# Performance work log

Hardware: AMD Instinct MI355X
Metric: run time of the kernel (lower is better)

Reference implementation:

```python
import jax, jax.numpy as jnp
import numpy as np

N_QUBITS = 14
LATENT = 14
DEPTH = 4
BATCH = 256
DIM = 1 << N_QUBITS  # 16384 amplitudes

# PennyLane convention: wire 0 is the most-significant bit of the flat state index.
_idx = np.arange(DIM)
_bits = (_idx[None, :] >> (N_QUBITS - 1 - np.arange(N_QUBITS)[:, None])) & 1  # [n_qubits, DIM]
_parity = np.sum(_bits[:-1] * _bits[1:], axis=0) % 2  # adjacent-pair CZ chain parity
CZ_SIGNS = jnp.asarray(1.0 - 2.0 * _parity, dtype=jnp.complex64)  # [DIM]
Z_SIGNS = jnp.asarray(1 - 2 * _bits[:LATENT], dtype=jnp.float32)  # [LATENT, DIM]


def _rx(t):
    c = jnp.cos(0.5 * t) + 0j
    s = -1j * jnp.sin(0.5 * t)
    m = jnp.stack([jnp.stack([c, s], -1), jnp.stack([s, c], -1)], -2)
    return m.astype(jnp.complex64)


def _ry(t):
    c = jnp.cos(0.5 * t)
    s = jnp.sin(0.5 * t)
    m = jnp.stack([jnp.stack([c, -s], -1), jnp.stack([s, c], -1)], -2)
    return m.astype(jnp.complex64)


def _rz(t):
    e = jnp.exp(-0.5j * t.astype(jnp.complex64))
    z = jnp.zeros_like(e)
    m = jnp.stack([jnp.stack([e, z], -1), jnp.stack([z, jnp.conj(e)], -1)], -2)
    return m.astype(jnp.complex64)


def _apply_1q(state, mat, wire):
    # state: [B, DIM]; mat: [2,2] (shared) or [B,2,2] (per-sample)
    B = state.shape[0]
    left = 1 << wire
    right = 1 << (N_QUBITS - wire - 1)
    st = state.reshape(B, left, 2, right)
    if mat.ndim == 3:
        st = jnp.einsum('bij,bajc->baic', mat, st)
    else:
        st = jnp.einsum('ij,bajc->baic', mat, st)
    return st.reshape(B, DIM)


def setup_inputs() -> dict:
    key = jax.random.key(0)
    k1, k2, k3, k4 = jax.random.split(key, 4)
    conditioning = jax.random.normal(k1, (BATCH, LATENT), dtype=jnp.float32)
    lim = 1.0 / np.sqrt(LATENT)
    W_enc = jax.random.uniform(k2, (N_QUBITS, LATENT), jnp.float32, -lim, lim)
    b_enc = jax.random.uniform(k3, (N_QUBITS,), jnp.float32, -lim, lim)
    # TorchLayer default init: U(0, 2*pi)
    weights = jax.random.uniform(k4, (DEPTH, N_QUBITS, 3), jnp.float32, 0.0, 2.0 * np.pi)
    return {"conditioning": conditioning, "W_enc": W_enc, "b_enc": b_enc, "weights": weights}


def reference(conditioning, W_enc, b_enc, weights):
    # encode: Linear + SiLU -> per-wire rotation angles [B, n_qubits]
    emb = conditioning @ W_enc.T + b_enc
    emb = emb * jax.nn.sigmoid(emb)
    B = emb.shape[0]

    state = jnp.zeros((B, DIM), jnp.complex64).at[:, 0].set(1.0)

    # angle encoding: RX(v) then RY(v) on each wire (per-sample gates)
    for w in range(N_QUBITS):
        v = emb[:, w]
        U = jnp.einsum('bij,bjk->bik', _ry(v), _rx(v))  # [B,2,2]
        state = _apply_1q(state, U, w)

    # variational layers: RZ, RX, RY per wire (shared gates), then CZ chain
    for d in range(DEPTH):
        for w in range(N_QUBITS):
            p = weights[d, w]
            U = _ry(p[2]) @ _rx(p[1]) @ _rz(p[0])  # [2,2]
            state = _apply_1q(state, U, w)
        state = state * CZ_SIGNS  # all adjacent CZs fused into one diagonal

    probs = state.real ** 2 + state.imag ** 2  # [B, DIM]
    latent = probs @ Z_SIGNS.T  # <Z_w> for w in range(LATENT) -> [B, LATENT]

    # F.layer_norm over last dim, no affine params
    mu = jnp.mean(latent, axis=-1, keepdims=True)
    var = jnp.var(latent, axis=-1, keepdims=True)
    return (latent - mu) / jnp.sqrt(var + 1e-5)
```

## Files before the change

### kernel.cpp

```cpp
#include <hip/hip_runtime.h>
#include <math.h>

#define NQ    14
#define DIM   16384
#define DEPTH 4

typedef __attribute__((ext_vector_type(2))) float f2;
typedef __attribute__((ext_vector_type(4))) float f4;

__device__ __forceinline__ f2 cmul(f2 a, f2 b) {
    return (f2){a.x*b.x - a.y*b.y, a.x*b.y + a.y*b.x};
}
__device__ __forceinline__ f2 cmac2(f2 x, f2 u, f2 us, f2 y, f2 v, f2 vs) {
    f2 r = x.xx * u;
    r += x.yy * us;
    r += y.xx * v;
    r += y.yy * vs;
    return r;
}


template<int CTRL>
__device__ __forceinline__ f2 dpp2(f2 v) {
    union U { f2 f; int i[2]; } u, r;
    u.f = v;
    r.i[0] = __builtin_amdgcn_update_dpp(0, u.i[0], CTRL, 0xF, 0xF, true);
    r.i[1] = __builtin_amdgcn_update_dpp(0, u.i[1], CTRL, 0xF, 0xF, true);
    return r.f;
}
template<int XB> __device__ __forceinline__ f2 lxchg(f2 v);
template<> __device__ __forceinline__ f2 lxchg<1>(f2 v) { return dpp2<0xB1>(v); }
template<> __device__ __forceinline__ f2 lxchg<2>(f2 v) { return dpp2<0x4E>(v); }
template<> __device__ __forceinline__ f2 lxchg<8>(f2 v) { return dpp2<0x128>(v); }

template<int MASK>
__device__ __forceinline__ void reg_gate(f2 a[16], const f4* G) {
    f4 g0 = G[0], g1 = G[1], g2 = G[2], g3 = G[3];
    #pragma unroll
    for (int l = 0; l < 16; ++l) {
        if (l & MASK) continue;
        const int j = l | MASK;
        f2 x = a[l], y = a[j];
        a[l] = cmac2(x, g0.xy, g0.zw, y, g1.xy, g1.zw);
        a[j] = cmac2(x, g2.xy, g2.zw, y, g3.xy, g3.zw);
    }
}

template<int XB>
__device__ __forceinline__ void lane_gate(f2 a[16], const f4* G, int t) {
    const bool hi = (t & XB) != 0;
    f4 c1 = G[hi ? 3 : 0];
    f4 c2 = G[hi ? 2 : 1];
    #pragma unroll
    for (int l = 0; l < 16; ++l) {
        f2 p = lxchg<XB>(a[l]);
        a[l] = cmac2(a[l], c1.xy, c1.zw, p, c2.xy, c2.zw);
    }
}

__device__ __forceinline__ void cz_A(f2 a[16], int t) {
    const int n = t & 63, w = t >> 6;
    const int pT = (__popc(w & (w >> 1)) + __popc(n & (n >> 1)) + ((n & 1) & (w >> 3))) & 1;
    const float F0 = pT ? -1.f : 1.f;
    const float F1 = (pT ^ ((n >> 5) & 1)) ? -1.f : 1.f;
    #pragma unroll
    for (int l = 0; l < 16; ++l) {
        float s = (l & 1) ? F1 : F0;
        if (__popc(l & (l >> 1)) & 1) s = -s;
        a[l] *= s;
    }
}

__device__ __forceinline__ void cz_B(f2 a[16], int t) {
    const int n = t & 63, w = t >> 6;
    const int n0 = n & 1, n1 = (n >> 1) & 1, n2 = (n >> 2) & 1;
    const int n3 = (n >> 3) & 1, n4 = (n >> 4) & 1, n5 = (n >> 5) & 1;
    const int pT = ((n2 & n4) ^ (n4 & n0) ^ (n0 & n5) ^ (n5 & n1) ^ (n1 & n3)
                    ^ (n3 & (w & 1)) ^ (__popc(w & (w >> 1)) & 1));
    const float F0 = pT ? -1.f : 1.f;
    const float F1 = (pT ^ n2) ? -1.f : 1.f;
    #pragma unroll
    for (int l = 0; l < 16; ++l) {
        float s = (l & 8) ? F1 : F0;
        if (__popc(l & (l >> 1)) & 1) s = -s;
        a[l] *= s;
    }
}

__global__ __launch_bounds__(1024)
void qlg_kernel(const float* __restrict__ cond,
                const float* __restrict__ Wenc,
                const float* __restrict__ benc,
                const float* __restrict__ wts,
                float* __restrict__ out)
{
    __shared__ f2 st[DIM];
    __shared__ f4 gates[DEPTH][NQ][4];
    __shared__ f2 qv[NQ][2];
    __shared__ f2 Phi[128];
    __shared__ f2 Plo[128];
    __shared__ float embS[NQ];
    __shared__ float wred[16][NQ];
    __shared__ float lat[NQ];

    const int b = blockIdx.x;
    const int t = threadIdx.x;
    const int n = t & 63, w = t >> 6;
    const int bB = (w << 10)
                 | (((n >> 3) & 1) << 5) | (((n >> 1) & 1) << 4)
                 | (((n >> 5) & 1) << 3) | ((n & 1) << 2)
                 | (((n >> 4) & 1) << 1) | ((n >> 2) & 1);

    if (t < NQ) {
        float s = benc[t];
        #pragma unroll
        for (int k = 0; k < NQ; ++k) s += cond[b*NQ + k] * Wenc[t*NQ + k];
        embS[t] = s / (1.0f + __expf(-s));
    }
    if (t >= 64 && t < 64 + DEPTH*NQ) {
        const int gi = t - 64;
        const int d = gi / NQ, ww = gi % NQ;
        const float p0 = wts[(d*NQ + ww)*3 + 0];
        const float p1 = wts[(d*NQ + ww)*3 + 1];
        const float p2 = wts[(d*NQ + ww)*3 + 2];
        float s0, c0, s1, c1, s2, c2;
        sincosf(0.5f*p0, &s0, &c0);
        sincosf(0.5f*p1, &s1, &c1);
        sincosf(0.5f*p2, &s2, &c2);
        f2 e0  = (f2){c0, -s0};
        f2 e0c = (f2){c0,  s0};
        f2 is1 = (f2){0.f, -s1};
        f2 m00 = c1 * e0;
        f2 m01 = cmul(is1, e0c);
        f2 m10 = cmul(is1, e0);
        f2 m11 = c1 * e0c;
        f2 u00 = c2*m00 - s2*m10;
        f2 u01 = c2*m01 - s2*m11;
        f2 u10 = s2*m00 + c2*m10;
        f2 u11 = s2*m01 + c2*m11;
        gates[d][ww][0] = (f4){u00.x, u00.y, -u00.y, u00.x};
        gates[d][ww][1] = (f4){u01.x, u01.y, -u01.y, u01.x};
        gates[d][ww][2] = (f4){u10.x, u10.y, -u10.y, u10.x};
        gates[d][ww][3] = (f4){u11.x, u11.y, -u11.y, u11.x};
    }
    __syncthreads();

    if (t < NQ) {
        float v = embS[t];
        float s, c;
        sincosf(0.5f*v, &s, &c);
        f2 a0 = (f2){c*c,  s*s};
        f2 a1 = (f2){s*c, -s*c};
        f2 u00 = gates[0][t][0].xy, u01 = gates[0][t][1].xy;
        f2 u10 = gates[0][t][2].xy, u11 = gates[0][t][3].xy;
        qv[t][0] = cmul(u00, a0) + cmul(u01, a1);
        qv[t][1] = cmul(u10, a0) + cmul(u11, a1);
    }
    __syncthreads();

    if (t < 128) {
        f2 p = qv[0][(t >> 6) & 1];
        #pragma unroll
        for (int ww = 1; ww <= 6; ++ww) p = cmul(p, qv[ww][(t >> (6 - ww)) & 1]);
        Phi[t] = p;
    } else if (t < 256) {
        const int j = t - 128;
        f2 p = qv[7][(j >> 6) & 1];
        #pragma unroll
        for (int ww = 8; ww <= 13; ++ww) p = cmul(p, qv[ww][(j >> (13 - ww)) & 1]);
        Plo[j] = p;
    }
    __syncthreads();

    f2 a[16];
    {
        f2 plo = Plo[((n & 7) << 4) | w];
        #pragma unroll
        for (int l = 0; l < 16; ++l)
            a[l] = cmul(Phi[(l << 3) | (n >> 3)], plo);
        cz_A(a, t);
    }

    {
        const f4 (*gl)[4] = gates[1];
        reg_gate<8>(a, gl[0]);
        reg_gate<4>(a, gl[1]);
        reg_gate<2>(a, gl[2]);
        reg_gate<1>(a, gl[3]);
        lane_gate<8>(a, gl[6], t);
        lane_gate<2>(a, gl[8], t);
        lane_gate<1>(a, gl[9], t);
    }

    #pragma unroll
    for (int l = 0; l < 16; ++l) st[t + (l << 10)] = a[l];
    __syncthreads();
    #pragma unroll
    for (int l = 0; l < 16; ++l) a[l] = st[bB + (l << 6)];

    {
        const f4 (*gl1)[4] = gates[1];
        reg_gate<8>(a, gl1[10]);
        reg_gate<4>(a, gl1[11]);
        reg_gate<2>(a, gl1[12]);
        reg_gate<1>(a, gl1[13]);
        lane_gate<8>(a, gl1[4], t);
        lane_gate<2>(a, gl1[5], t);
        lane_gate<1>(a, gl1[7], t);
        cz_B(a, t);
        const f4 (*gl2)[4] = gates[2];
        reg_gate<8>(a, gl2[10]);
        reg_gate<4>(a, gl2[11]);
        reg_gate<2>(a, gl2[12]);
        reg_gate<1>(a, gl2[13]);
        lane_gate<8>(a, gl2[4], t);
        lane_gate<2>(a, gl2[5], t);
        lane_gate<1>(a, gl2[7], t);
    }

    __syncthreads();
    #pragma unroll
    for (int l = 0; l < 16; ++l) st[bB + (l << 6)] = a[l];
    __syncthreads();
    #pragma unroll
    for (int l = 0; l < 16; ++l) a[l] = st[t + (l << 10)];

    {
        const f4 (*gl2)[4] = gates[2];
        reg_gate<8>(a, gl2[0]);
        reg_gate<4>(a, gl2[1]);
        reg_gate<2>(a, gl2[2]);
        reg_gate<1>(a, gl2[3]);
        lane_gate<8>(a, gl2[6], t);
        lane_gate<2>(a, gl2[8], t);
        lane_gate<1>(a, gl2[9], t);
        cz_A(a, t);
        const f4 (*gl3)[4] = gates[3];
        reg_gate<8>(a, gl3[0]);
        reg_gate<4>(a, gl3[1]);
        reg_gate<2>(a, gl3[2]);
        reg_gate<1>(a, gl3[3]);
        lane_gate<8>(a, gl3[6], t);
        lane_gate<2>(a, gl3[8], t);
        lane_gate<1>(a, gl3[9], t);
    }

    __syncthreads();
    #pragma unroll
    for (int l = 0; l < 16; ++l) st[t + (l << 10)] = a[l];
    __syncthreads();
    #pragma unroll
    for (int l = 0; l < 16; ++l) a[l] = st[bB + (l << 6)];

    float SU, Q10, Q11, Q12, Q13;
    {
        const f4 (*gl3)[4] = gates[3];
        reg_gate<8>(a, gl3[10]);
        reg_gate<4>(a, gl3[11]);
        reg_gate<2>(a, gl3[12]);
        reg_gate<1>(a, gl3[13]);
        lane_gate<8>(a, gl3[4], t);
        lane_gate<2>(a, gl3[5], t);
        lane_gate<1>(a, gl3[7], t);
        SU = Q10 = Q11 = Q12 = Q13 = 0.f;
        #pragma unroll
        for (int l = 0; l < 16; ++l) {
            float p = a[l].x*a[l].x + a[l].y*a[l].y;
            SU  += p;
            Q10 += (l & 8) ? -p : p;
            Q11 += (l & 4) ? -p : p;
            Q12 += (l & 2) ? -p : p;
            Q13 += (l & 1) ? -p : p;
        }
    }

    {
        const int lane = t & 63, wv = t >> 6;
        const int sbit[10] = {9, 8, 7, 6, 3, 1, 5, 0, 4, 2};
        #pragma unroll
        for (int ww = 0; ww < NQ; ++ww) {
            float v;
            if      (ww == 10) v = Q10;
            else if (ww == 11) v = Q11;
            else if (ww == 12) v = Q12;
            else if (ww == 13) v = Q13;
            else               v = ((t >> sbit[ww]) & 1) ? -SU : SU;
            #pragma unroll
            for (int off = 32; off > 0; off >>= 1) v += __shfl_down(v, off, 64);
            if (lane == 0) wred[wv][ww] = v;
        }
    }
    __syncthreads();
    if (t < NQ) {
        float s = 0.f;
        #pragma unroll
        for (int k = 0; k < 16; ++k) s += wred[k][t];
        lat[t] = s;
    }
    __syncthreads();
    if (t < NQ) {
        float mu = 0.f;
        #pragma unroll
        for (int k = 0; k < NQ; ++k) mu += lat[k];
        mu *= (1.0f / NQ);
        float var = 0.f;
        #pragma unroll
        for (int k = 0; k < NQ; ++k) { float dv = lat[k] - mu; var += dv*dv; }
        var *= (1.0f / NQ);
        out[b*NQ + t] = (lat[t] - mu) * rsqrtf(var + 1e-5f);
    }
}

extern "C" void kernel_launch(void* const* d_in, const int* in_sizes, int n_in,
                              void* d_out, int out_size, void* d_ws, size_t ws_size,
                              hipStream_t stream)
{
    (void)n_in; (void)d_ws; (void)ws_size; (void)out_size;
    const float* cond = (const float*)d_in[0];
    const float* Wenc = (const float*)d_in[1];
    const float* benc = (const float*)d_in[2];
    const float* wts  = (const float*)d_in[3];
    float* out = (float*)d_out;
    const int B = in_sizes[0] / NQ;
    qlg_kernel<<<dim3(B), dim3(1024), 0, stream>>>(cond, Wenc, benc, wts, out);
}
```

Measured before the change: 95.15 us.

## Split complex state into real/imag arrays and move gate coefficients to SGPRs

Stores amplitudes as separate real and imaginary float arrays. Gate matrices are compacted to two f4 per gate in shared memory and broadcast into scalar registers with readfirstlane. Each gate's loads are software-prefetched one gate ahead in a double-buffered pattern. The aim is to replace packed-vector complex MACs and per-gate LDS loads held in VGPRs with scalar-operand FMAs, cutting VGPR pressure and LDS latency stalls. This relies on the compiler actually keeping coefficients in SGPRs and may lose packed-FMA throughput.

```diff
diff --git a/kernel.cpp b/kernel.cpp
--- a/kernel.cpp
+++ b/kernel.cpp
@@ -11,54 +11,66 @@
 __device__ __forceinline__ f2 cmul(f2 a, f2 b) {
     return (f2){a.x*b.x - a.y*b.y, a.x*b.y + a.y*b.x};
 }
-__device__ __forceinline__ f2 cmac2(f2 x, f2 u, f2 us, f2 y, f2 v, f2 vs) {
-    f2 r = x.xx * u;
-    r += x.yy * us;
-    r += y.xx * v;
-    r += y.yy * vs;
-    return r;
-}
-
+
+__device__ __forceinline__ float rfl(float x) {
+    return __int_as_float(__builtin_amdgcn_readfirstlane(__float_as_int(x)));
+}
 
 template<int CTRL>
-__device__ __forceinline__ f2 dpp2(f2 v) {
-    union U { f2 f; int i[2]; } u, r;
-    u.f = v;
-    r.i[0] = __builtin_amdgcn_update_dpp(0, u.i[0], CTRL, 0xF, 0xF, true);
-    r.i[1] = __builtin_amdgcn_update_dpp(0, u.i[1], CTRL, 0xF, 0xF, true);
-    return r.f;
-}
-template<int XB> __device__ __forceinline__ f2 lxchg(f2 v);
-template<> __device__ __forceinline__ f2 lxchg<1>(f2 v) { return dpp2<0xB1>(v); }
-template<> __device__ __forceinline__ f2 lxchg<2>(f2 v) { return dpp2<0x4E>(v); }
-template<> __device__ __forceinline__ f2 lxchg<8>(f2 v) { return dpp2<0x128>(v); }
+__device__ __forceinline__ float dpp1(float v) {
+    return __int_as_float(__builtin_amdgcn_update_dpp(
+        0, __float_as_int(v), CTRL, 0xF, 0xF, true));
+}
+template<int XB> __device__ __forceinline__ float lx(float v);
+template<> __device__ __forceinline__ float lx<1>(float v) { return dpp1<0xB1>(v); }
+template<> __device__ __forceinline__ float lx<2>(float v) { return dpp1<0x4E>(v); }
+template<> __device__ __forceinline__ float lx<8>(float v) { return dpp1<0x128>(v); }
+
+
+struct GS {
+    float u00r,u00i,u01r,u01i,u10r,u10i,u11r,u11i;
+};
+__device__ __forceinline__ GS rflg(f4 va, f4 vb) {
+    GS g;
+    g.u00r = rfl(va.x); g.u00i = rfl(va.y);
+    g.u01r = rfl(va.z); g.u01i = rfl(va.w);
+    g.u10r = rfl(vb.x); g.u10i = rfl(vb.y);
+    g.u11r = rfl(vb.z); g.u11i = rfl(vb.w);
+    return g;
+}
 
 template<int MASK>
-__device__ __forceinline__ void reg_gate(f2 a[16], const f4* G) {
-    f4 g0 = G[0], g1 = G[1], g2 = G[2], g3 = G[3];
+__device__ __forceinline__ void reg_gate_s(float* ar, float* ai, const GS g) {
     #pragma unroll
     for (int l = 0; l < 16; ++l) {
         if (l & MASK) continue;
         const int j = l | MASK;
-        f2 x = a[l], y = a[j];
-        a[l] = cmac2(x, g0.xy, g0.zw, y, g1.xy, g1.zw);
-        a[j] = cmac2(x, g2.xy, g2.zw, y, g3.xy, g3.zw);
+        float xr = ar[l], xi = ai[l], yr = ar[j], yi = ai[j];
+        ar[l] = g.u00r*xr - g.u00i*xi + g.u01r*yr - g.u01i*yi;
+        ai[l] = g.u00r*xi + g.u00i*xr + g.u01r*yi + g.u01i*yr;
+        ar[j] = g.u10r*xr - g.u10i*xi + g.u11r*yr - g.u11i*yi;
+        ai[j] = g.u10r*xi + g.u10i*xr + g.u11r*yi + g.u11i*yr;
     }
 }
 
 template<int XB>
-__device__ __forceinline__ void lane_gate(f2 a[16], const f4* G, int t) {
+__device__ __forceinline__ void lane_gate_s(float* ar, float* ai, const GS g, int t) {
     const bool hi = (t & XB) != 0;
-    f4 c1 = G[hi ? 3 : 0];
-    f4 c2 = G[hi ? 2 : 1];
+    const float c1r = hi ? g.u11r : g.u00r;
+    const float c1i = hi ? g.u11i : g.u00i;
+    const float c2r = hi ? g.u10r : g.u01r;
+    const float c2i = hi ? g.u10i : g.u01i;
     #pragma unroll
     for (int l = 0; l < 16; ++l) {
-        f2 p = lxchg<XB>(a[l]);
-        a[l] = cmac2(a[l], c1.xy, c1.zw, p, c2.xy, c2.zw);
-    }
-}
-
-__device__ __forceinline__ void cz_A(f2 a[16], int t) {
+        float pr = lx<XB>(ar[l]);
+        float pi = lx<XB>(ai[l]);
+        float xr = ar[l], xi = ai[l];
+        ar[l] = c1r*xr - c1i*xi + c2r*pr - c2i*pi;
+        ai[l] = c1r*xi + c1i*xr + c2r*pi + c2i*pr;
+    }
+}
+
+__device__ __forceinline__ void cz_A(float* ar, float* ai, int t) {
     const int n = t & 63, w = t >> 6;
     const int pT = (__popc(w & (w >> 1)) + __popc(n & (n >> 1)) + ((n & 1) & (w >> 3))) & 1;
     const float F0 = pT ? -1.f : 1.f;
@@ -67,11 +79,11 @@
     for (int l = 0; l < 16; ++l) {
         float s = (l & 1) ? F1 : F0;
         if (__popc(l & (l >> 1)) & 1) s = -s;
-        a[l] *= s;
-    }
-}
-
-__device__ __forceinline__ void cz_B(f2 a[16], int t) {
+        ar[l] *= s; ai[l] *= s;
+    }
+}
+
+__device__ __forceinline__ void cz_B(float* ar, float* ai, int t) {
     const int n = t & 63, w = t >> 6;
     const int n0 = n & 1, n1 = (n >> 1) & 1, n2 = (n >> 2) & 1;
     const int n3 = (n >> 3) & 1, n4 = (n >> 4) & 1, n5 = (n >> 5) & 1;
@@ -83,7 +95,7 @@
     for (int l = 0; l < 16; ++l) {
         float s = (l & 8) ? F1 : F0;
         if (__popc(l & (l >> 1)) & 1) s = -s;
-        a[l] *= s;
+        ar[l] *= s; ai[l] *= s;
     }
 }
 
@@ -95,7 +107,7 @@
                 float* __restrict__ out)
 {
     __shared__ f2 st[DIM];
-    __shared__ f4 gates[DEPTH][NQ][4];
+    __shared__ f4 gatesL[DEPTH][NQ][2];
     __shared__ f2 qv[NQ][2];
     __shared__ f2 Phi[128];
     __shared__ f2 Plo[128];
@@ -138,10 +150,8 @@
         f2 u01 = c2*m01 - s2*m11;
         f2 u10 = s2*m00 + c2*m10;
         f2 u11 = s2*m01 + c2*m11;
-        gates[d][ww][0] = (f4){u00.x, u00.y, -u00.y, u00.x};
-        gates[d][ww][1] = (f4){u01.x, u01.y, -u01.y, u01.x};
-        gates[d][ww][2] = (f4){u10.x, u10.y, -u10.y, u10.x};
-        gates[d][ww][3] = (f4){u11.x, u11.y, -u11.y, u11.x};
+        gatesL[d][ww][0] = (f4){u00.x, u00.y, u01.x, u01.y};
+        gatesL[d][ww][1] = (f4){u10.x, u10.y, u11.x, u11.y};
     }
     __syncthreads();
 
@@ -151,8 +161,9 @@
         sincosf(0.5f*v, &s, &c);
         f2 a0 = (f2){c*c,  s*s};
         f2 a1 = (f2){s*c, -s*c};
-        f2 u00 = gates[0][t][0].xy, u01 = gates[0][t][1].xy;
-        f2 u10 = gates[0][t][2].xy, u11 = gates[0][t][3].xy;
+        f4 va = gatesL[0][t][0], vb = gatesL[0][t][1];
+        f2 u00 = (f2){va.x, va.y}, u01 = (f2){va.z, va.w};
+        f2 u10 = (f2){vb.x, vb.y}, u11 = (f2){vb.z, vb.w};
         qv[t][0] = cmul(u00, a0) + cmul(u01, a1);
         qv[t][1] = cmul(u10, a0) + cmul(u11, a1);
     }
@@ -172,100 +183,96 @@
     }
     __syncthreads();
 
-    f2 a[16];
+    float ar[16], ai[16];
     {
         f2 plo = Plo[((n & 7) << 4) | w];
         #pragma unroll
-        for (int l = 0; l < 16; ++l)
-            a[l] = cmul(Phi[(l << 3) | (n >> 3)], plo);
-        cz_A(a, t);
-    }
-
-    {
-        const f4 (*gl)[4] = gates[1];
-        reg_gate<8>(a, gl[0]);
-        reg_gate<4>(a, gl[1]);
-        reg_gate<2>(a, gl[2]);
-        reg_gate<1>(a, gl[3]);
-        lane_gate<8>(a, gl[6], t);
-        lane_gate<2>(a, gl[8], t);
-        lane_gate<1>(a, gl[9], t);
-    }
-
-    #pragma unroll
-    for (int l = 0; l < 16; ++l) st[t + (l << 10)] = a[l];
-    __syncthreads();
-    #pragma unroll
-    for (int l = 0; l < 16; ++l) a[l] = st[bB + (l << 6)];
-
-    {
-        const f4 (*gl1)[4] = gates[1];
-        reg_gate<8>(a, gl1[10]);
-        reg_gate<4>(a, gl1[11]);
-        reg_gate<2>(a, gl1[12]);
-        reg_gate<1>(a, gl1[13]);
-        lane_gate<8>(a, gl1[4], t);
-        lane_gate<2>(a, gl1[5], t);
-        lane_gate<1>(a, gl1[7], t);
-        cz_B(a, t);
-        const f4 (*gl2)[4] = gates[2];
-        reg_gate<8>(a, gl2[10]);
-        reg_gate<4>(a, gl2[11]);
-        reg_gate<2>(a, gl2[12]);
-        reg_gate<1>(a, gl2[13]);
-        lane_gate<8>(a, gl2[4], t);
-        lane_gate<2>(a, gl2[5], t);
-        lane_gate<1>(a, gl2[7], t);
-    }
-
-    __syncthreads();
-    #pragma unroll
-    for (int l = 0; l < 16; ++l) st[bB + (l << 6)] = a[l];
-    __syncthreads();
-    #pragma unroll
-    for (int l = 0; l < 16; ++l) a[l] = st[t + (l << 10)];
-
-    {
-        const f4 (*gl2)[4] = gates[2];
-        reg_gate<8>(a, gl2[0]);
-        reg_gate<4>(a, gl2[1]);
-        reg_gate<2>(a, gl2[2]);
-        reg_gate<1>(a, gl2[3]);
-        lane_gate<8>(a, gl2[6], t);
-        lane_gate<2>(a, gl2[8], t);
-        lane_gate<1>(a, gl2[9], t);
-        cz_A(a, t);
-        const f4 (*gl3)[4] = gates[3];
-        reg_gate<8>(a, gl3[0]);
-        reg_gate<4>(a, gl3[1]);
-        reg_gate<2>(a, gl3[2]);
-        reg_gate<1>(a, gl3[3]);
-        lane_gate<8>(a, gl3[6], t);
-        lane_gate<2>(a, gl3[8], t);
-        lane_gate<1>(a, gl3[9], t);
-    }
-
-    __syncthreads();
-    #pragma unroll
-    for (int l = 0; l < 16; ++l) st[t + (l << 10)] = a[l];
-    __syncthreads();
-    #pragma unroll
-    for (int l = 0; l < 16; ++l) a[l] = st[bB + (l << 6)];
+        for (int l = 0; l < 16; ++l) {
+            f2 ph = Phi[(l << 3) | (n >> 3)];
+            ar[l] = ph.x*plo.x - ph.y*plo.y;
+            ai[l] = ph.x*plo.y + ph.y*plo.x;
+        }
+        cz_A(ar, ai, t);
+    }
+
+    f4 va, vb, na, nb;
+    #define PREF(A_, B_, d_, q_) { A_ = gatesL[d_][q_][0]; B_ = gatesL[d_][q_][1]; }
+
+    PREF(va, vb, 1, 0);
+    PREF(na, nb, 1, 1); { GS G = rflg(va, vb); reg_gate_s<8>(ar, ai, G); }
+    PREF(va, vb, 1, 2); { GS G = rflg(na, nb); reg_gate_s<4>(ar, ai, G); }
+    PREF(na, nb, 1, 3); { GS G = rflg(va, vb); reg_gate_s<2>(ar, ai, G); }
+    PREF(va, vb, 1, 6); { GS G = rflg(na, nb); reg_gate_s<1>(ar, ai, G); }
+    PREF(na, nb, 1, 8); { GS G = rflg(va, vb); lane_gate_s<8>(ar, ai, G, t); }
+    PREF(va, vb, 1, 9); { GS G = rflg(na, nb); lane_gate_s<2>(ar, ai, G, t); }
+                        { GS G = rflg(va, vb); lane_gate_s<1>(ar, ai, G, t); }
+
+    #pragma unroll
+    for (int l = 0; l < 16; ++l) st[t + (l << 10)] = (f2){ar[l], ai[l]};
+    __syncthreads();
+    #pragma unroll
+    for (int l = 0; l < 16; ++l) { f2 v = st[bB + (l << 6)]; ar[l] = v.x; ai[l] = v.y; }
+
+    PREF(va, vb, 1, 10);
+    PREF(na, nb, 1, 11); { GS G = rflg(va, vb); reg_gate_s<8>(ar, ai, G); }
+    PREF(va, vb, 1, 12); { GS G = rflg(na, nb); reg_gate_s<4>(ar, ai, G); }
+    PREF(na, nb, 1, 13); { GS G = rflg(va, vb); reg_gate_s<2>(ar, ai, G); }
+    PREF(va, vb, 1, 4);  { GS G = rflg(na, nb); reg_gate_s<1>(ar, ai, G); }
+    PREF(na, nb, 1, 5);  { GS G = rflg(va, vb); lane_gate_s<8>(ar, ai, G, t); }
+    PREF(va, vb, 1, 7);  { GS G = rflg(na, nb); lane_gate_s<2>(ar, ai, G, t); }
+    PREF(na, nb, 2, 10); { GS G = rflg(va, vb); lane_gate_s<1>(ar, ai, G, t); }
+    cz_B(ar, ai, t);
+    PREF(va, vb, 2, 11); { GS G = rflg(na, nb); reg_gate_s<8>(ar, ai, G); }
+    PREF(na, nb, 2, 12); { GS G = rflg(va, vb); reg_gate_s<4>(ar, ai, G); }
+    PREF(va, vb, 2, 13); { GS G = rflg(na, nb); reg_gate_s<2>(ar, ai, G); }
+    PREF(na, nb, 2, 4);  { GS G = rflg(va, vb); reg_gate_s<1>(ar, ai, G); }
+    PREF(va, vb, 2, 5);  { GS G = rflg(na, nb); lane_gate_s<8>(ar, ai, G, t); }
+    PREF(na, nb, 2, 7);  { GS G = rflg(va, vb); lane_gate_s<2>(ar, ai, G, t); }
+                         { GS G = rflg(na, nb); lane_gate_s<1>(ar, ai, G, t); }
+
+    #pragma unroll
+    for (int l = 0; l < 16; ++l) st[bB + (l << 6)] = (f2){ar[l], ai[l]};
+    __syncthreads();
+    #pragma unroll
+    for (int l = 0; l < 16; ++l) { f2 v = st[t + (l << 10)]; ar[l] = v.x; ai[l] = v.y; }
+
+    PREF(va, vb, 2, 0);
+    PREF(na, nb, 2, 1); { GS G = rflg(va, vb); reg_gate_s<8>(ar, ai, G); }
+    PREF(va, vb, 2, 2); { GS G = rflg(na, nb); reg_gate_s<4>(ar, ai, G); }
+    PREF(na, nb, 2, 3); { GS G = rflg(va, vb); reg_gate_s<2>(ar, ai, G); }
+    PREF(va, vb, 2, 6); { GS G = rflg(na, nb); reg_gate_s<1>(ar, ai, G); }
+    PREF(na, nb, 2, 8); { GS G = rflg(va, vb); lane_gate_s<8>(ar, ai, G, t); }
+    PREF(va, vb, 2, 9); { GS G = rflg(na, nb); lane_gate_s<2>(ar, ai, G, t); }
+    PREF(na, nb, 3, 0); { GS G = rflg(va, vb); lane_gate_s<1>(ar, ai, G, t); }
+    cz_A(ar, ai, t);
+    PREF(va, vb, 3, 1); { GS G = rflg(na, nb); reg_gate_s<8>(ar, ai, G); }
+    PREF(na, nb, 3, 2); { GS G = rflg(va, vb); reg_gate_s<4>(ar, ai, G); }
+    PREF(va, vb, 3, 3); { GS G = rflg(na, nb); reg_gate_s<2>(ar, ai, G); }
+    PREF(na, nb, 3, 6); { GS G = rflg(va, vb); reg_gate_s<1>(ar, ai, G); }
+    PREF(va, vb, 3, 8); { GS G = rflg(na, nb); lane_gate_s<8>(ar, ai, G, t); }
+    PREF(na, nb, 3, 9); { GS G = rflg(va, vb); lane_gate_s<2>(ar, ai, G, t); }
+                        { GS G = rflg(na, nb); lane_gate_s<1>(ar, ai, G, t); }
+
+    #pragma unroll
+    for (int l = 0; l < 16; ++l) st[t + (l << 10)] = (f2){ar[l], ai[l]};
+    __syncthreads();
+    #pragma unroll
+    for (int l = 0; l < 16; ++l) { f2 v = st[bB + (l << 6)]; ar[l] = v.x; ai[l] = v.y; }
 
     float SU, Q10, Q11, Q12, Q13;
     {
-        const f4 (*gl3)[4] = gates[3];
-        reg_gate<8>(a, gl3[10]);
-        reg_gate<4>(a, gl3[11]);
-        reg_gate<2>(a, gl3[12]);
-        reg_gate<1>(a, gl3[13]);
-        lane_gate<8>(a, gl3[4], t);
-        lane_gate<2>(a, gl3[5], t);
-        lane_gate<1>(a, gl3[7], t);
+        PREF(va, vb, 3, 10);
+        PREF(na, nb, 3, 11); { GS G = rflg(va, vb); reg_gate_s<8>(ar, ai, G); }
+        PREF(va, vb, 3, 12); { GS G = rflg(na, nb); reg_gate_s<4>(ar, ai, G); }
+        PREF(na, nb, 3, 13); { GS G = rflg(va, vb); reg_gate_s<2>(ar, ai, G); }
+        PREF(va, vb, 3, 4);  { GS G = rflg(na, nb); reg_gate_s<1>(ar, ai, G); }
+        PREF(na, nb, 3, 5);  { GS G = rflg(va, vb); lane_gate_s<8>(ar, ai, G, t); }
+        PREF(va, vb, 3, 7);  { GS G = rflg(na, nb); lane_gate_s<2>(ar, ai, G, t); }
+                             { GS G = rflg(va, vb); lane_gate_s<1>(ar, ai, G, t); }
         SU = Q10 = Q11 = Q12 = Q13 = 0.f;
         #pragma unroll
         for (int l = 0; l < 16; ++l) {
-            float p = a[l].x*a[l].x + a[l].y*a[l].y;
+            float p = ar[l]*ar[l] + ai[l]*ai[l];
             SU  += p;
             Q10 += (l & 8) ? -p : p;
             Q11 += (l & 4) ? -p : p;
```

After: 134.7 us. 41.5% more time.
